# Optimization experiments

Measured on AMD Instinct MI355X. Metric: run time of the kernel, lower is better.

Reference implementation:

```python
import jax, jax.numpy as jnp
import numpy as np

B, T, F, H = 256, 256, 256, 256  # batch must equal hidden_size per the module's broadcasting


def _xavier(key, shape):
    fan_in, fan_out = shape
    lim = jnp.sqrt(6.0 / (fan_in + fan_out))
    return jax.random.uniform(key, shape, jnp.float32, -lim, lim)


def setup_inputs() -> dict:
    key = jax.random.key(0)
    ks = jax.random.split(key, 9)
    inp = {"x": jax.random.normal(ks[0], (B, T, F), jnp.float32)}
    names = ["ii", "hi", "if_", "hf", "ig", "hg", "io", "ho"]
    for i, n in enumerate(names):
        in_dim = F if n.startswith("i") else H
        inp[n + "_w"] = _xavier(ks[i + 1], (in_dim, H))
        inp[n + "_b"] = jnp.zeros((H,), jnp.float32)
    return inp


def reference(x, ii_w, ii_b, hi_w, hi_b, if__w, if__b, hf_w, hf_b,
              ig_w, ig_b, hg_w, hg_b, io_w, io_b, ho_w, ho_b):
    b = x.shape[0]
    h0 = jnp.zeros((H, H), x.dtype)
    c0 = jnp.zeros((H, H), x.dtype)
    # faithful to `for t in range(len(x)-1)`: len(x) == batch dim
    xs = jnp.moveaxis(x[:, : b - 1], 1, 0)  # (b-1, B, F)

    def step(carry, xt):
        h, c = carry
        i = jax.nn.sigmoid(xt @ ii_w + ii_b + h @ hi_w + hi_b)
        f = jax.nn.sigmoid(xt @ if__w + if__b + h @ hf_w + hf_b)
        g = jnp.tanh(xt @ ig_w + ig_b + h @ hg_w + hg_b)
        o = jax.nn.sigmoid(xt @ io_w + io_b + h @ ho_w + ho_b)
        c_new = f * c + i * g
        h_new = o * jnp.tanh(c_new)
        return (h_new, c_new), None

    (h, c), _ = jax.lax.scan(step, (h0, c0), xs)
    return h, c
```

## Files before the change

### kernel.cpp

```cpp
#include <hip/hip_runtime.h>


#define STEPS 255

typedef short bf16x8 __attribute__((ext_vector_type(8)));
typedef short bf16x4 __attribute__((ext_vector_type(4)));
typedef float f32x4  __attribute__((ext_vector_type(4)));

__device__ inline unsigned short f2bf(float f) {
  unsigned int u = __float_as_uint(f);
  unsigned int r = (u + 0x7FFFu + ((u >> 16) & 1u)) >> 16;
  return (unsigned short)r;
}
__device__ inline float bf2f(unsigned short s) {
  return __uint_as_float(((unsigned int)s) << 16);
}
__device__ inline float sig_f(float x) {
  float e = exp2f(-1.442695041f * x);
  return __builtin_amdgcn_rcpf(1.0f + e);
}
__device__ inline float tanh_f(float x) {
  float e = exp2f(-2.885390082f * x);
  return 2.0f * __builtin_amdgcn_rcpf(1.0f + e) - 1.0f;
}

__global__ __launch_bounds__(256) void lstm_prep_w(
    const float* __restrict__ m0, const float* __restrict__ m1,
    const float* __restrict__ m2, const float* __restrict__ m3,
    const float* __restrict__ m4, const float* __restrict__ m5,
    const float* __restrict__ m6, const float* __restrict__ m7,
    unsigned short* __restrict__ WxT, unsigned short* __restrict__ WhT) {
  const float* mats[8] = {m0, m1, m2, m3, m4, m5, m6, m7};
  int mat = blockIdx.z;
  const float* W = mats[mat];
  unsigned short* out = (mat < 4 ? WxT : WhT) + (size_t)(mat & 3) * 256 * 256;
  int kblk = blockIdx.x * 32, jblk = blockIdx.y * 32;
  __shared__ float tile[32][33];
  int tx = threadIdx.x & 31, ty = threadIdx.x >> 5;
#pragma unroll
  for (int i = 0; i < 4; ++i) {
    int kk = ty + i * 8;
    tile[kk][tx] = W[(size_t)(kblk + kk) * 256 + jblk + tx];
  }
  __syncthreads();
#pragma unroll
  for (int i = 0; i < 4; ++i) {
    int jj = ty + i * 8;
    out[(size_t)(jblk + jj) * 256 + kblk + tx] = f2bf(tile[tx][jj]);
  }
}

__global__ void lstm_prep_b(
    const float* __restrict__ bx0, const float* __restrict__ bx1,
    const float* __restrict__ bx2, const float* __restrict__ bx3,
    const float* __restrict__ bh0, const float* __restrict__ bh1,
    const float* __restrict__ bh2, const float* __restrict__ bh3,
    float* __restrict__ bcat) {
  const float* bx[4] = {bx0, bx1, bx2, bx3};
  const float* bh[4] = {bh0, bh1, bh2, bh3};
  int i = blockIdx.x * 256 + threadIdx.x;
  int g = i >> 8, j = i & 255;
  bcat[i] = bx[g][j] + bh[g][j];
}

__global__ __launch_bounds__(256, 1) void lstm_precompute(
    const float* __restrict__ x, const unsigned short* __restrict__ WxT,
    const float* __restrict__ bcat, unsigned short* __restrict__ P) {
  int t = blockIdx.x;
  int tid = threadIdx.x;
  int w = tid >> 6, lane = tid & 63, q = lane >> 4, cl = lane & 15;
  int rbase = w * 64;

  bf16x8 bfrag[8][4];
#pragma unroll
  for (int kt = 0; kt < 8; ++kt) {
    int k0 = kt * 32 + q * 8;
#pragma unroll
    for (int rt = 0; rt < 4; ++rt) {
      const float* xp = x + (((size_t)(rbase + rt * 16 + cl) * 256 + t) * 256 + k0);
      f32x4 lo = *(const f32x4*)xp;
      f32x4 hi = *(const f32x4*)(xp + 4);
      bf16x8 bv;
      bv[0] = (short)f2bf(lo[0]); bv[1] = (short)f2bf(lo[1]);
      bv[2] = (short)f2bf(lo[2]); bv[3] = (short)f2bf(lo[3]);
      bv[4] = (short)f2bf(hi[0]); bv[5] = (short)f2bf(hi[1]);
      bv[6] = (short)f2bf(hi[2]); bv[7] = (short)f2bf(hi[3]);
      bfrag[kt][rt] = bv;
    }
  }

  for (int nbi = 0; nbi < 8; ++nbi) {
    int nblk = (blockIdx.y * 8 + nbi) * 64;
    f32x4 acc[4][4];
#pragma unroll
    for (int a = 0; a < 4; ++a)
#pragma unroll
      for (int b = 0; b < 4; ++b) acc[a][b] = f32x4{0.f, 0.f, 0.f, 0.f};

#pragma unroll
    for (int kt = 0; kt < 8; ++kt) {
      int k0 = kt * 32 + q * 8;
      bf16x8 afrag[4];
#pragma unroll
      for (int mt = 0; mt < 4; ++mt)
        afrag[mt] = *(const bf16x8*)(WxT + (size_t)(nblk + mt * 16 + cl) * 256 + k0);
#pragma unroll
      for (int mt = 0; mt < 4; ++mt)
#pragma unroll
        for (int rt = 0; rt < 4; ++rt)
          acc[mt][rt] = __builtin_amdgcn_mfma_f32_16x16x32_bf16(
              afrag[mt], bfrag[kt][rt], acc[mt][rt], 0, 0, 0);
    }
#pragma unroll
    for (int mt = 0; mt < 4; ++mt) {
#pragma unroll
      for (int reg = 0; reg < 4; ++reg) {
        int n = nblk + mt * 16 + q * 4 + reg;
        float bb = bcat[n];
#pragma unroll
        for (int rt = 0; rt < 4; ++rt) {
          int rg16 = w * 4 + rt;
          P[(((size_t)t * 16 + rg16) * 1024 + n) * 16 + cl] = f2bf(acc[mt][rt][reg] + bb);
        }
      }
    }
  }
}

__global__ __launch_bounds__(512, 2) void lstm_recurrent(
    const unsigned short* __restrict__ WhT,
    const unsigned short* __restrict__ P,
    float* __restrict__ out) {
  __shared__ bf16x8 o_w[8][2][8][64];
  __shared__ unsigned short hbuf[2][16 * 256];

  int tid = threadIdx.x;
  int w = tid >> 6, lane = tid & 63, q = lane >> 4, cl = lane & 15;
  int b_ = blockIdx.x;
  int x = (b_ & 7) * 16 + (b_ >> 3);
  int rg16 = x >> 3;
  int idxb = (x & 7) * 2;

  for (int i = 0; i < 16; ++i) {
    int idx = tid + i * 512;
    int sw = idx >> 10, sb = (idx >> 9) & 1, skt = (idx >> 6) & 7, sl = idx & 63;
    int sq = sl >> 4, scl = sl & 15;
    int col = (2 * sw + sb) * 16 + scl;
    int k0 = skt * 32 + sq * 8;
    o_w[sw][sb][skt][sl] = *(const bf16x8*)(WhT + (size_t)(3 * 256 + col) * 256 + k0);
  }

  bf16x8 wreg[2][3][8];
#pragma unroll
  for (int b = 0; b < 2; ++b)
#pragma unroll
    for (int g = 0; g < 3; ++g)
#pragma unroll
      for (int kt = 0; kt < 8; ++kt) {
        int col = (2 * w + b) * 16 + cl;
        wreg[b][g][kt] =
            *(const bf16x8*)(WhT + (size_t)(g * 256 + col) * 256 + kt * 32 + q * 8);
      }

  for (int i = tid; i < 4096; i += 512) ((unsigned int*)&hbuf[0][0])[i] = 0;

  asm volatile("" ::: "memory");
  __syncthreads();

  int abase = cl * 512 + ((q * 16) ^ ((cl & 7) << 4));

  int bq = q >> 1, rq = q & 1;
  int colq = 32 * w + bq * 16 + cl;
  int idx15 = idxb + rq;

  float creg = 0.f;

  for (int t = 0; t < STEPS; ++t) {
    int rb = t & 1;
    bool lastt = (t == STEPS - 1);
    const unsigned short* hr = &hbuf[rb][0];
    unsigned short* hw = &hbuf[rb ^ 1][0];

    unsigned short pv[4];
    {
      const unsigned short* pp =
          P + (((size_t)t * 16 + rg16) * 1024 + colq) * 16 + idx15;
#pragma unroll
      for (int g = 0; g < 4; ++g) pv[g] = pp[(size_t)g * 4096];
    }

    f32x4 acc[2][4];
#pragma unroll
    for (int b = 0; b < 2; ++b)
#pragma unroll
      for (int g = 0; g < 4; ++g) acc[b][g] = f32x4{0.f, 0.f, 0.f, 0.f};

#pragma unroll
    for (int kt = 0; kt < 8; ++kt) {
      bf16x8 af = *(const bf16x8*)(hr + ((abase ^ (kt * 64)) >> 1));
      acc[0][0] = __builtin_amdgcn_mfma_f32_16x16x32_bf16(af, wreg[0][0][kt], acc[0][0], 0, 0, 0);
      acc[0][1] = __builtin_amdgcn_mfma_f32_16x16x32_bf16(af, wreg[0][1][kt], acc[0][1], 0, 0, 0);
      acc[0][2] = __builtin_amdgcn_mfma_f32_16x16x32_bf16(af, wreg[0][2][kt], acc[0][2], 0, 0, 0);
      acc[0][3] = __builtin_amdgcn_mfma_f32_16x16x32_bf16(af, o_w[w][0][kt][lane], acc[0][3], 0, 0, 0);
      acc[1][0] = __builtin_amdgcn_mfma_f32_16x16x32_bf16(af, wreg[1][0][kt], acc[1][0], 0, 0, 0);
      acc[1][1] = __builtin_amdgcn_mfma_f32_16x16x32_bf16(af, wreg[1][1][kt], acc[1][1], 0, 0, 0);
      acc[1][2] = __builtin_amdgcn_mfma_f32_16x16x32_bf16(af, wreg[1][2][kt], acc[1][2], 0, 0, 0);
      acc[1][3] = __builtin_amdgcn_mfma_f32_16x16x32_bf16(af, o_w[w][1][kt][lane], acc[1][3], 0, 0, 0);
    }

    float sh1[4], sh2[4], sh3[4], ag[4];
#pragma unroll
    for (int g = 0; g < 4; ++g) {
      sh1[g] = __shfl_xor(acc[0][g][1], 16, 64);
      sh2[g] = __shfl_xor(acc[1][g][0], 32, 64);
      sh3[g] = __shfl_xor(acc[1][g][1], 48, 64);
    }
#pragma unroll
    for (int g = 0; g < 4; ++g)
      ag[g] = (q == 0) ? acc[0][g][0]
            : (q == 1) ? sh1[g]
            : (q == 2) ? sh2[g]
                       : sh3[g];

    {
      float pi = ag[0] + bf2f(pv[0]);
      float pf = ag[1] + bf2f(pv[1]);
      float pg = ag[2] + bf2f(pv[2]);
      float po = ag[3] + bf2f(pv[3]);
      float ig = sig_f(pi), fg = sig_f(pf), gg = tanh_f(pg), og = sig_f(po);
      float cn = fg * creg + ig * gg;
      creg = cn;
      float hn = og * tanh_f(cn);
      if (!lastt) {
        int wb = rq * 512 + ((colq * 2) ^ (rq << 4));
        hw[wb >> 1] = f2bf(hn);
      } else {
        out[(size_t)(x * 2 + rq) * 256 + colq] = hn;
        out[65536 + (size_t)(x * 2 + rq) * 256 + colq] = cn;
      }
    }

    __syncthreads();
  }
}

extern "C" void kernel_launch(void* const* d_in, const int* in_sizes, int n_in,
                              void* d_out, int out_size, void* d_ws, size_t ws_size,
                              hipStream_t stream) {
  const float* x = (const float*)d_in[0];
  const float* wx0 = (const float*)d_in[1];
  const float* wx1 = (const float*)d_in[5];
  const float* wx2 = (const float*)d_in[9];
  const float* wx3 = (const float*)d_in[13];
  const float* wh0 = (const float*)d_in[3];
  const float* wh1 = (const float*)d_in[7];
  const float* wh2 = (const float*)d_in[11];
  const float* wh3 = (const float*)d_in[15];
  const float* bx0 = (const float*)d_in[2];
  const float* bx1 = (const float*)d_in[6];
  const float* bx2 = (const float*)d_in[10];
  const float* bx3 = (const float*)d_in[14];
  const float* bh0 = (const float*)d_in[4];
  const float* bh1 = (const float*)d_in[8];
  const float* bh2 = (const float*)d_in[12];
  const float* bh3 = (const float*)d_in[16];

  char* ws = (char*)d_ws;
  unsigned short* WxT = (unsigned short*)(ws + 0);
  unsigned short* WhT = (unsigned short*)(ws + 524288);
  float* bcat = (float*)(ws + 1048576);
  unsigned short* P = (unsigned short*)(ws + 1052672);

  lstm_prep_w<<<dim3(8, 8, 8), 256, 0, stream>>>(wx0, wx1, wx2, wx3,
                                                 wh0, wh1, wh2, wh3, WxT, WhT);
  lstm_prep_b<<<4, 256, 0, stream>>>(bx0, bx1, bx2, bx3, bh0, bh1, bh2, bh3, bcat);
  lstm_precompute<<<dim3(255, 2), 256, 0, stream>>>(x, WxT, bcat, P);
  lstm_recurrent<<<dim3(128), 512, 0, stream>>>(WhT, P, (float*)d_out);
}
```

Before: 822.0 us.

## Keep output-gate weights in registers and shrink hidden-state LDS buffer to active rows

Moves the output-gate recurrent weights from LDS into per-thread registers, removing per-step LDS reads of those weight fragments. Shrinks the hidden-state double buffer to only the two rows actually used, and has only lanes with cl<2 load the A fragment while the rest feed zeros. This cuts LDS traffic and footprint in the serial recurrence but adds 64 VGPRs of weights, which may cause spills at launch bounds of 512 threads with 2 blocks per CU. The unseen write-back code must match the new 512-element buffer layout.

```diff
diff --git a/kernel.cpp b/kernel.cpp
--- a/kernel.cpp
+++ b/kernel.cpp
@@ -131,8 +131,7 @@
     const unsigned short* __restrict__ WhT,
     const unsigned short* __restrict__ P,
     float* __restrict__ out) {
-  __shared__ bf16x8 o_w[8][2][8][64];
-  __shared__ unsigned short hbuf[2][16 * 256];
+  __shared__ unsigned short hbuf[2][512];
 
   int tid = threadIdx.x;
   int w = tid >> 6, lane = tid & 63, q = lane >> 4, cl = lane & 15;
@@ -141,33 +140,30 @@
   int rg16 = x >> 3;
   int idxb = (x & 7) * 2;
 
-  for (int i = 0; i < 16; ++i) {
-    int idx = tid + i * 512;
-    int sw = idx >> 10, sb = (idx >> 9) & 1, skt = (idx >> 6) & 7, sl = idx & 63;
-    int sq = sl >> 4, scl = sl & 15;
-    int col = (2 * sw + sb) * 16 + scl;
-    int k0 = skt * 32 + sq * 8;
-    o_w[sw][sb][skt][sl] = *(const bf16x8*)(WhT + (size_t)(3 * 256 + col) * 256 + k0);
-  }
-
   bf16x8 wreg[2][3][8];
-#pragma unroll
-  for (int b = 0; b < 2; ++b)
+  bf16x8 oreg[2][8];
+#pragma unroll
+  for (int b = 0; b < 2; ++b) {
+    int col = (2 * w + b) * 16 + cl;
 #pragma unroll
     for (int g = 0; g < 3; ++g)
 #pragma unroll
-      for (int kt = 0; kt < 8; ++kt) {
-        int col = (2 * w + b) * 16 + cl;
+      for (int kt = 0; kt < 8; ++kt)
         wreg[b][g][kt] =
             *(const bf16x8*)(WhT + (size_t)(g * 256 + col) * 256 + kt * 32 + q * 8);
-      }
-
-  for (int i = tid; i < 4096; i += 512) ((unsigned int*)&hbuf[0][0])[i] = 0;
+#pragma unroll
+    for (int kt = 0; kt < 8; ++kt)
+      oreg[b][kt] =
+          *(const bf16x8*)(WhT + (size_t)(3 * 256 + col) * 256 + kt * 32 + q * 8);
+  }
+
+  for (int i = tid; i < 512; i += 512) ((unsigned int*)&hbuf[0][0])[i] = 0;
 
   asm volatile("" ::: "memory");
   __syncthreads();
 
   int abase = cl * 512 + ((q * 16) ^ ((cl & 7) << 4));
+  bool ard = (cl < 2);
 
   int bq = q >> 1, rq = q & 1;
   int colq = 32 * w + bq * 16 + cl;
@@ -189,6 +185,14 @@
       for (int g = 0; g < 4; ++g) pv[g] = pp[(size_t)g * 4096];
     }
 
+    bf16x8 af[8];
+#pragma unroll
+    for (int kt = 0; kt < 8; ++kt) {
+      bf16x8 z = {0, 0, 0, 0, 0, 0, 0, 0};
+      if (ard) z = *(const bf16x8*)(hr + ((abase ^ (kt * 64)) >> 1));
+      af[kt] = z;
+    }
+
     f32x4 acc[2][4];
 #pragma unroll
     for (int b = 0; b < 2; ++b)
@@ -197,15 +201,14 @@
 
 #pragma unroll
     for (int kt = 0; kt < 8; ++kt) {
-      bf16x8 af = *(const bf16x8*)(hr + ((abase ^ (kt * 64)) >> 1));
-      acc[0][0] = __builtin_amdgcn_mfma_f32_16x16x32_bf16(af, wreg[0][0][kt], acc[0][0], 0, 0, 0);
-      acc[0][1] = __builtin_amdgcn_mfma_f32_16x16x32_bf16(af, wreg[0][1][kt], acc[0][1], 0, 0, 0);
-      acc[0][2] = __builtin_amdgcn_mfma_f32_16x16x32_bf16(af, wreg[0][2][kt], acc[0][2], 0, 0, 0);
-      acc[0][3] = __builtin_amdgcn_mfma_f32_16x16x32_bf16(af, o_w[w][0][kt][lane], acc[0][3], 0, 0, 0);
-      acc[1][0] = __builtin_amdgcn_mfma_f32_16x16x32_bf16(af, wreg[1][0][kt], acc[1][0], 0, 0, 0);
-      acc[1][1] = __builtin_amdgcn_mfma_f32_16x16x32_bf16(af, wreg[1][1][kt], acc[1][1], 0, 0, 0);
-      acc[1][2] = __builtin_amdgcn_mfma_f32_16x16x32_bf16(af, wreg[1][2][kt], acc[1][2], 0, 0, 0);
-      acc[1][3] = __builtin_amdgcn_mfma_f32_16x16x32_bf16(af, o_w[w][1][kt][lane], acc[1][3], 0, 0, 0);
+      acc[0][0] = __builtin_amdgcn_mfma_f32_16x16x32_bf16(af[kt], wreg[0][0][kt], acc[0][0], 0, 0, 0);
+      acc[0][1] = __builtin_amdgcn_mfma_f32_16x16x32_bf16(af[kt], wreg[0][1][kt], acc[0][1], 0, 0, 0);
+      acc[0][2] = __builtin_amdgcn_mfma_f32_16x16x32_bf16(af[kt], wreg[0][2][kt], acc[0][2], 0, 0, 0);
+      acc[0][3] = __builtin_amdgcn_mfma_f32_16x16x32_bf16(af[kt], oreg[0][kt],    acc[0][3], 0, 0, 0);
+      acc[1][0] = __builtin_amdgcn_mfma_f32_16x16x32_bf16(af[kt], wreg[1][0][kt], acc[1][0], 0, 0, 0);
+      acc[1][1] = __builtin_amdgcn_mfma_f32_16x16x32_bf16(af[kt], wreg[1][1][kt], acc[1][1], 0, 0, 0);
+      acc[1][2] = __builtin_amdgcn_mfma_f32_16x16x32_bf16(af[kt], wreg[1][2][kt], acc[1][2], 0, 0, 0);
+      acc[1][3] = __builtin_amdgcn_mfma_f32_16x16x32_bf16(af[kt], oreg[1][kt],    acc[1][3], 0, 0, 0);
     }
 
     float sh1[4], sh2[4], sh3[4], ag[4];
```

Measured after the change: 1.842 ms. +124.1%, slower.

## Split recurrent LSTM across 256 blocks with one batch row per block

Applied to the files above, without the earlier changes.

The recurrent kernel now launches 256 blocks, each owning a single batch row instead of two. The h buffer shrinks to one row, padded so that each group of four lanes reads the same data. Only half of the lanes (q<2) keep cell state and write results, which removes two of the three cross-lane shuffles. The P pointer is hoisted out of the loop and advanced each step. The intent is to shorten the per-step serial work and use more CUs, at the cost of reloading the full weight set in twice as many blocks and running MFMAs whose rows are mostly redundant.

```diff
diff --git a/kernel.cpp b/kernel.cpp
--- a/kernel.cpp
+++ b/kernel.cpp
@@ -132,14 +132,14 @@
     const unsigned short* __restrict__ P,
     float* __restrict__ out) {
   __shared__ bf16x8 o_w[8][2][8][64];
-  __shared__ unsigned short hbuf[2][16 * 256];
+  __shared__ unsigned short hbuf[2][1152];
 
   int tid = threadIdx.x;
   int w = tid >> 6, lane = tid & 63, q = lane >> 4, cl = lane & 15;
   int b_ = blockIdx.x;
-  int x = (b_ & 7) * 16 + (b_ >> 3);
-  int rg16 = x >> 3;
-  int idxb = (x & 7) * 2;
+  int x = (b_ & 7) * 32 + (b_ >> 3);
+  int rg16 = x >> 4;
+  int idx15 = x & 15;
 
   for (int i = 0; i < 16; ++i) {
     int idx = tid + i * 512;
@@ -162,32 +162,30 @@
             *(const bf16x8*)(WhT + (size_t)(g * 256 + col) * 256 + kt * 32 + q * 8);
       }
 
-  for (int i = tid; i < 4096; i += 512) ((unsigned int*)&hbuf[0][0])[i] = 0;
+  for (int i = tid; i < 1152; i += 512) ((unsigned int*)&hbuf[0][0])[i] = 0;
 
   asm volatile("" ::: "memory");
   __syncthreads();
 
-  int abase = cl * 512 + ((q * 16) ^ ((cl & 7) << 4));
-
-  int bq = q >> 1, rq = q & 1;
-  int colq = 32 * w + bq * 16 + cl;
-  int idx15 = idxb + rq;
+  int abase = (cl & 3) * 576 + q * 16;
+
+  int qe = q & 1;
+  int colq = 32 * w + qe * 16 + cl;
+  bool own = (q < 2);
 
   float creg = 0.f;
+  const unsigned short* pp = P + ((size_t)rg16 * 1024 + colq) * 16 + idx15;
 
   for (int t = 0; t < STEPS; ++t) {
     int rb = t & 1;
     bool lastt = (t == STEPS - 1);
-    const unsigned short* hr = &hbuf[rb][0];
+    const char* hr = (const char*)&hbuf[rb][0];
     unsigned short* hw = &hbuf[rb ^ 1][0];
 
     unsigned short pv[4];
-    {
-      const unsigned short* pp =
-          P + (((size_t)t * 16 + rg16) * 1024 + colq) * 16 + idx15;
-#pragma unroll
-      for (int g = 0; g < 4; ++g) pv[g] = pp[(size_t)g * 4096];
-    }
+#pragma unroll
+    for (int g = 0; g < 4; ++g) pv[g] = pp[(size_t)g * 4096];
+    pp += (size_t)16 * 1024 * 16;
 
     f32x4 acc[2][4];
 #pragma unroll
@@ -197,7 +195,7 @@
 
 #pragma unroll
     for (int kt = 0; kt < 8; ++kt) {
-      bf16x8 af = *(const bf16x8*)(hr + ((abase ^ (kt * 64)) >> 1));
+      bf16x8 af = *(const bf16x8*)(hr + abase + kt * 64);
       acc[0][0] = __builtin_amdgcn_mfma_f32_16x16x32_bf16(af, wreg[0][0][kt], acc[0][0], 0, 0, 0);
       acc[0][1] = __builtin_amdgcn_mfma_f32_16x16x32_bf16(af, wreg[0][1][kt], acc[0][1], 0, 0, 0);
       acc[0][2] = __builtin_amdgcn_mfma_f32_16x16x32_bf16(af, wreg[0][2][kt], acc[0][2], 0, 0, 0);
@@ -208,19 +206,11 @@
       acc[1][3] = __builtin_amdgcn_mfma_f32_16x16x32_bf16(af, o_w[w][1][kt][lane], acc[1][3], 0, 0, 0);
     }
 
-    float sh1[4], sh2[4], sh3[4], ag[4];
-#pragma unroll
-    for (int g = 0; g < 4; ++g) {
-      sh1[g] = __shfl_xor(acc[0][g][1], 16, 64);
-      sh2[g] = __shfl_xor(acc[1][g][0], 32, 64);
-      sh3[g] = __shfl_xor(acc[1][g][1], 48, 64);
-    }
-#pragma unroll
-    for (int g = 0; g < 4; ++g)
-      ag[g] = (q == 0) ? acc[0][g][0]
-            : (q == 1) ? sh1[g]
-            : (q == 2) ? sh2[g]
-                       : sh3[g];
+    float sh[4], ag[4];
+#pragma unroll
+    for (int g = 0; g < 4; ++g) sh[g] = __shfl_xor(acc[1][g][0], 16, 64);
+#pragma unroll
+    for (int g = 0; g < 4; ++g) ag[g] = (q == 0) ? acc[0][g][0] : sh[g];
 
     {
       float pi = ag[0] + bf2f(pv[0]);
@@ -229,14 +219,15 @@
       float po = ag[3] + bf2f(pv[3]);
       float ig = sig_f(pi), fg = sig_f(pf), gg = tanh_f(pg), og = sig_f(po);
       float cn = fg * creg + ig * gg;
-      creg = cn;
+      creg = own ? cn : creg;
       float hn = og * tanh_f(cn);
-      if (!lastt) {
-        int wb = rq * 512 + ((colq * 2) ^ (rq << 4));
-        hw[wb >> 1] = f2bf(hn);
-      } else {
-        out[(size_t)(x * 2 + rq) * 256 + colq] = hn;
-        out[65536 + (size_t)(x * 2 + rq) * 256 + colq] = cn;
+      if (own) {
+        if (!lastt) {
+          hw[colq] = f2bf(hn);
+        } else {
+          out[(size_t)x * 256 + colq] = hn;
+          out[65536 + (size_t)x * 256 + colq] = cn;
+        }
       }
     }
 
@@ -275,5 +266,5 @@
                                                  wh0, wh1, wh2, wh3, WxT, WhT);
   lstm_prep_b<<<4, 256, 0, stream>>>(bx0, bx1, bx2, bx3, bh0, bh1, bh2, bh3, bcat);
   lstm_precompute<<<dim3(255, 2), 256, 0, stream>>>(x, WxT, bcat, P);
-  lstm_recurrent<<<dim3(128), 512, 0, stream>>>(WhT, P, (float*)d_out);
-}
+  lstm_recurrent<<<dim3(256), 512, 0, stream>>>(WhT, P, (float*)d_out);
+}
```

Measured after the change: 862.2 us. +4.9%, slower.
